# Optimization experiments

Measured on AMD Instinct MI355X. Metric: run time of the kernel, lower is better.

## Reference

```python
import jax, jax.numpy as jnp
import numpy as np

B_, L_, H_ = 2, 2048, 2048          # batch, seq_len, hidden_size
I_, N_, NH, P_ = 4096, 128, 64, 64   # intermediate, ssm_state, num_heads, head_dim
K_, CH = 4, 256                      # conv kernel, chunk size
DT_MIN, DT_MAX = 0.0, 1e10


def setup_inputs() -> dict:
    key = jax.random.key(0)
    ks = jax.random.split(key, 8)
    conv_dim = I_ + 2 * N_
    proj_out = 2 * (I_ + N_) + NH
    return {
        "hidden_states": jax.random.normal(ks[0], (B_, L_, H_), jnp.float32),
        "W_in": jax.random.normal(ks[1], (proj_out, H_), jnp.float32) * 0.02,
        "conv_w": jax.random.normal(ks[2], (conv_dim, 1, K_), jnp.float32) * 0.2,
        "conv_b": jnp.zeros((conv_dim,), jnp.float32),
        "dt_bias": jax.random.uniform(ks[3], (NH,), jnp.float32),
        "A_log": jnp.log(jax.random.uniform(ks[4], (NH,), jnp.float32, 1.0, 16.0)),
        "D": jnp.ones((NH,), jnp.float32),
        "norm_w": jnp.ones((I_,), jnp.float32),
        "W_out": jax.random.normal(ks[5], (H_, I_), jnp.float32) * 0.02,
    }


def _segsum(x):
    # stable segment-sum: out[..., i, j] = sum_{k=j+1..i} x[..., k] for i>=j, else -inf
    T = x.shape[-1]
    xr = jnp.broadcast_to(x[..., None], x.shape + (T,))
    lower = jnp.tril(jnp.ones((T, T), bool), -1)
    s = jnp.cumsum(jnp.where(lower, xr, 0.0), axis=-2)
    return jnp.where(jnp.tril(jnp.ones((T, T), bool)), s, -jnp.inf)


def reference(hidden_states, W_in, conv_w, conv_b, dt_bias, A_log, D, norm_w, W_out):
    b, L, _ = hidden_states.shape
    proj = hidden_states @ W_in.T                       # (b, L, 2*(I+N)+H)
    z, xBC, dt = jnp.split(proj, [I_, 2 * I_ + 2 * N_], axis=-1)

    # depthwise causal conv1d + silu
    x_t = xBC.transpose(0, 2, 1)                        # (b, conv_dim, L)
    conv = jax.lax.conv_general_dilated(
        x_t, conv_w, (1,), [(K_ - 1, 0)],
        dimension_numbers=("NCH", "OIH", "NCH"), feature_group_count=I_ + 2 * N_)
    xBC = jax.nn.silu((conv + conv_b[None, :, None]).transpose(0, 2, 1))
    x, Bm, Cm = jnp.split(xBC, [I_, I_ + N_], axis=-1)  # (b,L,I) (b,L,N) (b,L,N)

    # ---- SSD naive (chunked state-space-duality scan) ----
    A = -jnp.exp(A_log.astype(jnp.float32))             # (h,)
    dt = jnp.clip(jax.nn.softplus(dt + dt_bias), DT_MIN, DT_MAX)  # (b,L,h)
    x4 = x.reshape(b, L, NH, P_)
    pad = (-L) % CH
    padf = lambda t: jnp.pad(t, [(0, 0), (0, pad)] + [(0, 0)] * (t.ndim - 2))
    D_res = D[None, None, :, None] * padf(x4)           # (b, Lp, h, p)
    xs = padf(x4 * dt[..., None])
    Ah = padf(A[None, None, :] * dt)                    # (b, Lp, h)
    Bc, Cc = padf(Bm), padf(Cm)
    c = (L + pad) // CH
    xs = xs.reshape(b, c, CH, NH, P_)                   # (b,c,l,h,p)
    Ah = Ah.reshape(b, c, CH, NH).transpose(0, 3, 1, 2) # (b,h,c,l)
    Bc = Bc.reshape(b, c, CH, N_)
    Cc = Cc.reshape(b, c, CH, N_)

    A_cs = jnp.cumsum(Ah, axis=-1)                      # (b,h,c,l)
    Lm = jnp.exp(_segsum(Ah))                           # (b,h,c,l,l)
    # intra-chunk (diagonal block) output; B/C shared across heads (n_groups=1)
    Y_diag = jnp.einsum("bcln,bcsn,bhcls,bcshp->bclhp", Cc, Bc, Lm, xs)

    decay_states = jnp.exp(A_cs[..., -1:] - A_cs)       # (b,h,c,l)
    states = jnp.einsum("bcln,bhcl,bclhp->bchpn", Bc, decay_states, xs)
    states = jnp.concatenate([jnp.zeros_like(states[:, :1]), states], axis=1)
    decay_chunk = jnp.exp(_segsum(jnp.pad(A_cs[..., -1], [(0, 0), (0, 0), (1, 0)])))
    new_states = jnp.einsum("bhzc,bchpn->bzhpn", decay_chunk, states)
    states = new_states[:, :-1]                         # (b,c,h,p,n)
    Y_off = jnp.einsum("bcln,bchpn,bhcl->bclhp", Cc, states, jnp.exp(A_cs))

    y = (Y_diag + Y_off).reshape(b, c * CH, NH, P_) + D_res
    y = y[:, :L].reshape(b, L, I_)

    # gated RMSNorm (normalize=True: multiply by silu(residual) before norm)
    yf = y.astype(jnp.float32) * jax.nn.silu(z.astype(jnp.float32))
    yf = yf * jax.lax.rsqrt(jnp.mean(yf * yf, -1, keepdims=True) + 1e-5) * norm_w
    return yf.astype(hidden_states.dtype) @ W_out.T
```

## Files before the change

kernel.cpp:

```cpp
#include <hip/hip_runtime.h>
#include <hip/hip_bf16.h>
#include <math.h>


#define B_SZ 2
#define L_SZ 2048
#define H_SZ 2048
#define I_SZ 4096
#define N_SZ 128
#define NH_SZ 64
#define P_SZ 64
#define CH_SZ 256
#define NC_SZ 8
#define PROJ_SZ 8512
#define CONV_SZ 4352
#define XOFF 4096
#define DTOFF 8448
#define BOFF 4096
#define COFF 4224

typedef __attribute__((ext_vector_type(8))) short short8_t;
typedef __attribute__((ext_vector_type(4))) float float4_t;

#define GLDS(gp, lp)                                                   \
// ... 82 lines not shown
                           f2bf(b.x), f2bf(b.y), f2bf(b.z), f2bf(b.w)};
    *(uint4*)(dst + e) = *(const uint4*)o;
  } else {
    *(uint4*)(dst + e) = *(const uint4*)((const unsigned short*)src + e);
  }
}

#define MFMA_ACC(d, a, b) \
  d = __builtin_amdgcn_mfma_f32_16x16x32_bf16(a, b, d, 0, 0, 0)
#define LDA_FR(buf, i, kk) \
  (*(const short8_t*)&As[(buf)*16384 + (wm*128 + (i)*16 + l16)*64 + \
                         (((((kk)<<2) + quad) ^ l7) << 3)])
#define LDB_FR(buf, j, kk) \
  (*(const short8_t*)&Bs[(buf)*16384 + (wn*64 + (j)*16 + l16)*64 + \
                         (((((kk)<<2) + quad) ^ l7) << 3)])
#define STAGE_A(h, tile, buf) do {                                          \
    GLDS(aSrc[h][0] + ((long long)(tile) << 6),                             \
         &As[(buf)*16384 + (h)*8192 + (wave*16)*64]);                       \
    GLDS(aSrc[h][1] + ((long long)(tile) << 6),                             \
         &As[(buf)*16384 + (h)*8192 + (wave*16 + 8)*64]);                   \
  } while (0)
#define STAGE_B(h, tile, buf) do {                                          \
    GLDS(bSrc[h][0] + ((long long)(tile) << 6),                             \
         &Bs[(buf)*16384 + (h)*8192 + (wave*16)*64]);                       \
    GLDS(bSrc[h][1] + ((long long)(tile) << 6),                             \
         &Bs[(buf)*16384 + (h)*8192 + (wave*16 + 8)*64]);                   \
  } while (0)

__global__ __launch_bounds__(512, 2)
void gemm_8ph_k(const unsigned short* __restrict__ A,
                const unsigned short* __restrict__ B,
                unsigned short* __restrict__ C,
                int N, int K, int lda, int ldb, int ldc, int gxTiles) {
  __shared__ alignas(16) unsigned short As[2 * 256 * 64];
  __shared__ alignas(16) unsigned short Bs[2 * 256 * 64];
  const int t = threadIdx.x;
  const int lane = t & 63;
  const int wave = t >> 6;
  const int quad = lane >> 4;
  const int l16 = lane & 15;
  const int l7 = lane & 7;
  const int l3 = lane >> 3;
  const int wm = wave >> 2;
  const int wn = wave & 3;

  int id = blockIdx.x;
  const int nwg = gridDim.x;
  int swz = id;
  if ((nwg & 7) == 0) swz = (id & 7) * (nwg >> 3) + (id >> 3);
  const int band = gxTiles << 2;
  const int by = (swz & 3) + ((swz / band) << 2);
  const int bx = (swz >> 2) % gxTiles;
  const int m0 = by << 8;
  const int n0 = bx << 8;
  const int NT = K >> 6;

  const int kperm = ((l7 ^ l3) << 3);
  const unsigned short* aSrc[2][2];
  const unsigned short* bSrc[2][2];
#pragma unroll
  for (int h = 0; h < 2; ++h)
#pragma unroll
    for (int c = 0; c < 2; ++c) {
      const int rloc = h * 128 + wave * 16 + c * 8 + l3;
      aSrc[h][c] = A + (long long)(m0 + rloc) * lda + kperm;
      int bn = n0 + rloc;
      if (bn > N - 1) bn = N - 1;
      bSrc[h][c] = B + (long long)bn * ldb + kperm;
    }

  float4_t acc[8][4];
#pragma unroll
  for (int i = 0; i < 8; ++i)
#pragma unroll
    for (int j = 0; j < 4; ++j) acc[i][j] = (float4_t){0.f, 0.f, 0.f, 0.f};

  STAGE_A(0, 0, 0); STAGE_A(1, 0, 0);
  STAGE_B(0, 0, 0); STAGE_B(1, 0, 0);
  STAGE_B(0, 1, 1); STAGE_B(1, 1, 1);
  asm volatile("s_waitcnt vmcnt(4)" ::: "memory");
  __builtin_amdgcn_s_barrier();

  short8_t af[4][2], bf[4][2];
  for (int tt = 0; tt < NT; ++tt) {
    const int rb = tt & 1, nb = rb ^ 1;
#pragma unroll
    for (int i = 0; i < 4; ++i) af[i][0] = LDA_FR(rb, i, 0);
#pragma unroll
    for (int j = 0; j < 4; ++j) bf[j][0] = LDB_FR(rb, j, 0);
    if (tt + 1 < NT) STAGE_A(0, tt + 1, nb);
    asm volatile("s_waitcnt lgkmcnt(4)" ::: "memory");
    __builtin_amdgcn_s_barrier();
    asm volatile("s_waitcnt lgkmcnt(0)" ::: "memory");
    __builtin_amdgcn_s_setprio(1);
#pragma unroll
    for (int i = 0; i < 4; ++i)
#pragma unroll
      for (int j = 0; j < 4; ++j) MFMA_ACC(acc[i][j], af[i][0], bf[j][0]);
    __builtin_amdgcn_s_setprio(0);
    __builtin_amdgcn_s_barrier();
#pragma unroll
    for (int i = 0; i < 4; ++i) af[i][1] = LDA_FR(rb, i, 1);
#pragma unroll
    for (int j = 0; j < 4; ++j) bf[j][1] = LDB_FR(rb, j, 1);
    if (tt + 1 < NT) STAGE_A(1, tt + 1, nb);
    asm volatile("s_waitcnt lgkmcnt(4)" ::: "memory");
    __builtin_amdgcn_s_barrier();
    asm volatile("s_waitcnt lgkmcnt(0)" ::: "memory");
    __builtin_amdgcn_s_setprio(1);
#pragma unroll
    for (int i = 0; i < 4; ++i)
#pragma unroll
      for (int j = 0; j < 4; ++j) MFMA_ACC(acc[i][j], af[i][1], bf[j][1]);
    __builtin_amdgcn_s_setprio(0);
    __builtin_amdgcn_s_barrier();
#pragma unroll
    for (int i = 0; i < 4; ++i) af[i][0] = LDA_FR(rb, 4 + i, 0);
    if (tt + 2 < NT) STAGE_B(0, tt + 2, rb);
    __builtin_amdgcn_s_barrier();
    asm volatile("s_waitcnt lgkmcnt(0)" ::: "memory");
    __builtin_amdgcn_s_setprio(1);
#pragma unroll
    for (int i = 0; i < 4; ++i)
#pragma unroll
      for (int j = 0; j < 4; ++j) MFMA_ACC(acc[4 + i][j], af[i][0], bf[j][0]);
    __builtin_amdgcn_s_setprio(0);
    __builtin_amdgcn_s_barrier();
#pragma unroll
    for (int i = 0; i < 4; ++i) af[i][1] = LDA_FR(rb, 4 + i, 1);
    if (tt + 2 < NT) STAGE_B(1, tt + 2, rb);
    __builtin_amdgcn_s_barrier();
    asm volatile("s_waitcnt lgkmcnt(0)" ::: "memory");
    __builtin_amdgcn_s_setprio(1);
#pragma unroll
    for (int i = 0; i < 4; ++i)
#pragma unroll
      for (int j = 0; j < 4; ++j) MFMA_ACC(acc[4 + i][j], af[i][1], bf[j][1]);
    __builtin_amdgcn_s_setprio(0);
    if (tt < NT - 2) asm volatile("s_waitcnt vmcnt(4)" ::: "memory");
    else             asm volatile("s_waitcnt vmcnt(0)" ::: "memory");
    __builtin_amdgcn_s_barrier();
  }

#pragma unroll
  for (int i = 0; i < 8; ++i) {
#pragma unroll
    for (int r = 0; r < 4; ++r) {
      const int m = m0 + wm * 128 + i * 16 + quad * 4 + r;
      const long long cb = (long long)m * ldc;
#pragma unroll
      for (int j = 0; j < 4; ++j) {
        const int n = n0 + wn * 64 + j * 16 + l16;
        if (n < N) C[cb + n] = f2bf(acc[i][j][r]);
      }
    }
  }
}

template <int OUT_MODE>
__global__ __launch_bounds__(256)
void gemm_dma_k(const unsigned short* __restrict__ A,
                const unsigned short* __restrict__ B,
                void* __restrict__ Cptr, int M, int N, int K,
                int lda, int ldb, int ldc,
                const int* __restrict__ flags, int fo) {
  __shared__ unsigned short As[128 * 32];
  __shared__ unsigned short Bs[128 * 32];
  const int t = threadIdx.x;
  const int lane = t & 63;
  const int wave = t >> 6;
  const int quad = lane >> 4;
  const int l16 = lane & 15;
  int bx = blockIdx.x, by = blockIdx.y;
  {
    const int nwg = gridDim.x * gridDim.y;
    if ((nwg & 7) == 0 && (gridDim.y & 3) == 0) {
      int id = blockIdx.y * gridDim.x + blockIdx.x;
      int swz = (id & 7) * (nwg >> 3) + (id >> 3);
      by = (swz & 3) + ((swz / (gridDim.x << 2)) << 2);
      bx = (swz >> 2) % gridDim.x;
    }
  }
  const int m0 = by * 128, n0 = bx * 128;
  const int wm = (wave >> 1) * 64, wn = (wave & 1) * 64;
  const int ofp = (OUT_MODE == 2) ? flags[fo] : 0;

  float4_t acc[4][4];
#pragma unroll
  for (int i = 0; i < 4; i++)
#pragma unroll
    for (int j = 0; j < 4; j++) acc[i][j] = (float4_t){0.f, 0.f, 0.f, 0.f};

  const int rr = lane >> 2;
  const int ks = (lane & 3) * 8;
  const long long aR0 = (long long)(m0 + wave * 16 + rr) * lda + ks;
  const long long aR1 = aR0 + (long long)64 * lda;
  const long long bR0 = (long long)(n0 + wave * 16 + rr) * ldb + ks;
  const long long bR1 = bR0 + (long long)64 * ldb;
  unsigned short* asd0 = &As[(wave * 16) * 32];
  unsigned short* asd1 = &As[(64 + wave * 16) * 32];
  unsigned short* bsd0 = &Bs[(wave * 16) * 32];
  unsigned short* bsd1 = &Bs[(64 + wave * 16) * 32];

  for (int k0 = 0; k0 < K; k0 += 32) {
    __syncthreads();
    GLDS(A + aR0 + k0, asd0);
    GLDS(A + aR1 + k0, asd1);
    GLDS(B + bR0 + k0, bsd0);
    GLDS(B + bR1 + k0, bsd1);
    __syncthreads();
    short8_t afr[4], bfr[4];
#pragma unroll
    for (int i = 0; i < 4; i++)
      afr[i] = *(const short8_t*)&As[(wm + i * 16 + l16) * 32 + quad * 8];
#pragma unroll
    for (int j = 0; j < 4; j++)
      bfr[j] = *(const short8_t*)&Bs[(wn + j * 16 + l16) * 32 + quad * 8];
#pragma unroll
    for (int i = 0; i < 4; i++)
#pragma unroll
      for (int j = 0; j < 4; j++)
        acc[i][j] = __builtin_amdgcn_mfma_f32_16x16x32_bf16(
            afr[i], bfr[j], acc[i][j], 0, 0, 0);
  }
#pragma unroll
  for (int i = 0; i < 4; i++) {
#pragma unroll
    for (int r = 0; r < 4; r++) {
      const int m = m0 + wm + i * 16 + quad * 4 + r;
      const long long base = (long long)m * ldc;
#pragma unroll
      for (int j = 0; j < 4; j++) {
        const int n = n0 + wn + j * 16 + l16;
        if (n < N) {
          float v = acc[i][j][r];
          if (ofp) ((float*)Cptr)[base + n] = v;
          else     ((unsigned short*)Cptr)[base + n] = f2bf(v);
        }
      }
    }
  }
}

template <int OUT_MODE>
__global__ __launch_bounds__(256)
void gemm_bt_k(const void* __restrict__ A, const void* __restrict__ B,
               void* __restrict__ Cptr, int M, int N, int K,
               int lda, int ldb, int ldc,
               long long sA, long long sB, long long sC,
               const int* __restrict__ flags, int fa, int fb, int fo) {
  __shared__ float As[128][20];
  __shared__ float Bs[128][20];
  const int t = threadIdx.x;
  const int tx = t & 15, ty = t >> 4;
  const int m0 = blockIdx.y * 128, n0 = blockIdx.x * 128;
  const int afp = flags[fa], bfp = flags[fb];
  const int ofp = (OUT_MODE == 2) ? flags[fo] : (OUT_MODE == 1);
  const long long zoff = (long long)blockIdx.z;
  float* Cf = (float*)Cptr + zoff * sC;
  unsigned short* Cb = (unsigned short*)Cptr + zoff * sC;

  float acc[8][8];
#pragma unroll
  for (int i = 0; i < 8; i++)
#pragma unroll
    for (int j = 0; j < 8; j++) acc[i][j] = 0.f;

  const int rowS = t >> 1;
  const int kof  = (t & 1) * 8;
  const long long aRow = zoff * sA + (long long)(m0 + rowS) * lda + kof;
  const long long bRow = zoff * sB + (long long)(n0 + rowS) * ldb + kof;
  const bool bOK = (n0 + rowS) < N;

  for (int k0 = 0; k0 < K; k0 += 16) {
    float af[8], bf[8];
    load8(A, aRow + k0, afp, af);
    if (bOK) load8(B, bRow + k0, bfp, bf);
    else { bf[0]=bf[1]=bf[2]=bf[3]=bf[4]=bf[5]=bf[6]=bf[7]=0.f; }
    __syncthreads();
    *(float4*)&As[rowS][kof]     = make_float4(af[0], af[1], af[2], af[3]);
    *(float4*)&As[rowS][kof + 4] = make_float4(af[4], af[5], af[6], af[7]);
    *(float4*)&Bs[rowS][kof]     = make_float4(bf[0], bf[1], bf[2], bf[3]);
    *(float4*)&Bs[rowS][kof + 4] = make_float4(bf[4], bf[5], bf[6], bf[7]);
    __syncthreads();
#pragma unroll
    for (int kk = 0; kk < 16; kk += 2) {
      float2 a2[8], b2[8];
#pragma unroll
      for (int i = 0; i < 8; i++) a2[i] = *(const float2*)&As[ty + 16 * i][kk];
#pragma unroll
      for (int j = 0; j < 8; j++) b2[j] = *(const float2*)&Bs[tx + 16 * j][kk];
#pragma unroll
      for (int i = 0; i < 8; i++)
#pragma unroll
        for (int j = 0; j < 8; j++) {
          acc[i][j] = fmaf(a2[i].x, b2[j].x, acc[i][j]);
          acc[i][j] = fmaf(a2[i].y, b2[j].y, acc[i][j]);
        }
    }
  }
#pragma unroll
  for (int i = 0; i < 8; i++) {
    const int m = m0 + ty + 16 * i;
    const long long base = (long long)m * ldc;
#pragma unroll
    for (int j = 0; j < 8; j++) {
      const int n = n0 + tx + 16 * j;
      if (n < N) {
        if (ofp) Cf[base + n] = acc[i][j];
        else     Cb[base + n] = f2bf(acc[i][j]);
      }
    }
  }
}

__global__ __launch_bounds__(256)
void conv_silu_k(const unsigned short* __restrict__ proj,
                 const void* __restrict__ cw,
                 const void* __restrict__ cb,
                 unsigned short* __restrict__ convx,
                 const int* __restrict__ flags) {
  const int total = B_SZ * L_SZ * (CONV_SZ / 4);
  int g = blockIdx.x * 256 + threadIdx.x;
  if (g >= total) return;
  const int fw = flags[2], fb = flags[3];
  int c4 = g % (CONV_SZ / 4);
  int bl = g / (CONV_SZ / 4);
  int l = bl & (L_SZ - 1);
  int ch = c4 * 4;
  float w0[8], w1[8];
  load8(cw, (long long)ch * 4, fw, w0);
  load8(cw, (long long)ch * 4 + 8, fw, w1);
  float accv[4];
  load4(cb, ch, fb, accv);
  float acc0 = accv[0], acc1 = accv[1], acc2 = accv[2], acc3 = accv[3];
  const long long rb = (long long)(bl - l);
#pragma unroll
  for (int k = 0; k < 4; k++) {
    int ls = l - 3 + k;
    if (ls < 0) continue;
    uint2 xv = *(const uint2*)(proj + (rb + ls) * PROJ_SZ + XOFF + ch);
    float x0 = bf2f((unsigned short)(xv.x & 0xffffu));
    float x1 = bf2f((unsigned short)(xv.x >> 16));
    float x2 = bf2f((unsigned short)(xv.y & 0xffffu));
    float x3 = bf2f((unsigned short)(xv.y >> 16));
    acc0 = fmaf(x0, w0[k], acc0);
    acc1 = fmaf(x1, w0[4 + k], acc1);
    acc2 = fmaf(x2, w1[k], acc2);
    acc3 = fmaf(x3, w1[4 + k], acc3);
  }
  unsigned short o0 = f2bf(silu_f(acc0));
  unsigned short o1 = f2bf(silu_f(acc1));
  unsigned short o2 = f2bf(silu_f(acc2));
  unsigned short o3 = f2bf(silu_f(acc3));
  *(uint2*)(convx + (long long)bl * CONV_SZ + ch) =
      make_uint2((unsigned int)o0 | ((unsigned int)o1 << 16),
                 (unsigned int)o2 | ((unsigned int)o3 << 16));
}

__global__ __launch_bounds__(256)
void dt_prep_k(const unsigned short* __restrict__ proj,
               const void* __restrict__ dt_bias,
               float* __restrict__ dtv, const int* __restrict__ flags) {
  int g = blockIdx.x * 256 + threadIdx.x;
  int h = g & 63;
  long long bl = g >> 6;
  float v = bf2f(proj[bl * PROJ_SZ + DTOFF + h]) + load1(dt_bias, h, flags[4]);
  float sp = (v > 20.f) ? v : log1pf(expf(v));
  dtv[g] = sp;
}

__global__ __launch_bounds__(256)
void acs_scan_k(const float* __restrict__ dtv,
                const void* __restrict__ A_log,
                float* __restrict__ acs, const int* __restrict__ flags) {
  __shared__ float sd[256];
  int blk = blockIdx.x;
  int h = blk & 63;
  int bc = blk >> 6;
  int l = threadIdx.x;
  float Ah = -expf(load1(A_log, h, flags[5]));
  long long row = (long long)bc * CH_SZ + l;
  sd[l] = Ah * dtv[row * NH_SZ + h];
  for (int off = 1; off < 256; off <<= 1) {
    __syncthreads();
    float tv = (l >= off) ? sd[l - off] : 0.f;
    __syncthreads();
    sd[l] += tv;
  }
  acs[(long long)blk * CH_SZ + l] = sd[l];
}

__global__ __launch_bounds__(256)
void chunk_states_k(const unsigned short* __restrict__ convx,
                    const float* __restrict__ dtv,
                    const float* __restrict__ acs,
                    float* __restrict__ stc) {
  __shared__ float Bw[32][128];
  __shared__ float xw[32][64];
  int blk = blockIdx.x;
  int h = blk & 63;
  int bc = blk >> 6;
  int t = threadIdx.x;
  const int p0 = (t & 15) * 4, n0 = (t >> 4) * 8;
  const float* acsb = acs + (long long)blk * 256;
  const float alast = acsb[255];
  float acc[4][8];
#pragma unroll
  for (int i = 0; i < 4; i++)
#pragma unroll
    for (int j = 0; j < 8; j++) acc[i][j] = 0.f;
  const long long row0 = (long long)bc * 256;

  for (int lt0 = 0; lt0 < 256; lt0 += 32) {
    __syncthreads();
#pragma unroll
    for (int q = 0; q < 4; q++) {
      int idx4 = (t + 256 * q) * 4;
      int r = idx4 >> 7, n = idx4 & 127;
      uint2 v = *(const uint2*)(convx + (row0 + lt0 + r) * CONV_SZ + BOFF + n);
      Bw[r][n]     = bf2f((unsigned short)(v.x & 0xffffu));
      Bw[r][n + 1] = bf2f((unsigned short)(v.x >> 16));
      Bw[r][n + 2] = bf2f((unsigned short)(v.y & 0xffffu));
      Bw[r][n + 3] = bf2f((unsigned short)(v.y >> 16));
    }
#pragma unroll
    for (int q = 0; q < 2; q++) {
      int idx4 = (t + 256 * q) * 4;
      int r = idx4 >> 6, p = idx4 & 63;
      long long lg = row0 + lt0 + r;
      float sc = dtv[lg * NH_SZ + h] * expf(alast - acsb[lt0 + r]);
      uint2 v = *(const uint2*)(convx + lg * CONV_SZ + h * 64 + p);
      xw[r][p]     = bf2f((unsigned short)(v.x & 0xffffu)) * sc;
      xw[r][p + 1] = bf2f((unsigned short)(v.x >> 16)) * sc;
      xw[r][p + 2] = bf2f((unsigned short)(v.y & 0xffffu)) * sc;
      xw[r][p + 3] = bf2f((unsigned short)(v.y >> 16)) * sc;
    }
    __syncthreads();
#pragma unroll 4
    for (int lt = 0; lt < 32; lt++) {
      float4 xv = *(const float4*)&xw[lt][p0];
      float4 b0 = *(const float4*)&Bw[lt][n0];
      float4 b1 = *(const float4*)&Bw[lt][n0 + 4];
      float xa[4] = {xv.x, xv.y, xv.z, xv.w};
      float ba[8] = {b0.x, b0.y, b0.z, b0.w, b1.x, b1.y, b1.z, b1.w};
#pragma unroll
      for (int i = 0; i < 4; i++)
#pragma unroll
        for (int j = 0; j < 8; j++) acc[i][j] = fmaf(xa[i], ba[j], acc[i][j]);
    }
  }
  float* outb = stc + (long long)blk * 8192;
#pragma unroll
  for (int i = 0; i < 4; i++) {
    *(float4*)&outb[(p0 + i) * 128 + n0] =
        make_float4(acc[i][0], acc[i][1], acc[i][2], acc[i][3]);
    *(float4*)&outb[(p0 + i) * 128 + n0 + 4] =
        make_float4(acc[i][4], acc[i][5], acc[i][6], acc[i][7]);
  }
}

__global__ __launch_bounds__(256)
void recur_k(float* __restrict__ stc, const float* __restrict__ acs) {
  int blk = blockIdx.x;
  int b = blk >> 6, h = blk & 63;
  int t = threadIdx.x;
  float S[32];
#pragma unroll
  for (int j = 0; j < 32; j++) S[j] = 0.f;
  for (int z = 0; z < 8; z++) {
    long long bz = ((long long)b * 8 + z) * 64 + h;
    long long base = bz * 8192;
    float e = expf(acs[bz * 256 + 255]);
#pragma unroll
    for (int j = 0; j < 32; j++) {
      int idx = j * 256 + t;
      float cs = stc[base + idx];
      stc[base + idx] = S[j];
      S[j] = fmaf(e, S[j], cs);
    }
  }
}

__global__ __launch_bounds__(256)
void yoff_k(const unsigned short* __restrict__ convx,
            const float* __restrict__ sti,
            const float* __restrict__ acs,
            const void* __restrict__ Dw,
            float* __restrict__ y, const int* __restrict__ flags) {
  __shared__ float SIt[128][68];
  __shared__ unsigned short Ct[64][128];
  int blk = blockIdx.x;
  int h = blk & 63;
  int bc = blk >> 6;
  int t = threadIdx.x;
  const int txp = t & 15, lq = t >> 4;
  const float Dh = load1(Dw, h, flags[6]);
  const float* sib = sti + (long long)blk * 8192;
#pragma unroll 4
  for (int q = 0; q < 32; q++) {
    int idx = t + 256 * q;
    SIt[idx & 127][idx >> 7] = sib[idx];
  }
  const float* acsb = acs + (long long)blk * 256;
  const long long row0 = (long long)bc * 256;
  for (int ltile = 0; ltile < 4; ltile++) {
    __syncthreads();
#pragma unroll 4
    for (int q = 0; q < 32; q++) {
      int idx = t + 256 * q;
      int lr = idx >> 7, n = idx & 127;
      Ct[lr][n] = convx[(row0 + ltile * 64 + lr) * CONV_SZ + COFF + n];
    }
    __syncthreads();
    float acc[4][4] = {};
#pragma unroll 4
    for (int n = 0; n < 128; n++) {
      float4 sv = *(const float4*)&SIt[n][txp * 4];
      float c0 = bf2f(Ct[lq * 4 + 0][n]);
      float c1 = bf2f(Ct[lq * 4 + 1][n]);
      float c2 = bf2f(Ct[lq * 4 + 2][n]);
      float c3 = bf2f(Ct[lq * 4 + 3][n]);
      acc[0][0] = fmaf(c0, sv.x, acc[0][0]); acc[0][1] = fmaf(c0, sv.y, acc[0][1]);
      acc[0][2] = fmaf(c0, sv.z, acc[0][2]); acc[0][3] = fmaf(c0, sv.w, acc[0][3]);
      acc[1][0] = fmaf(c1, sv.x, acc[1][0]); acc[1][1] = fmaf(c1, sv.y, acc[1][1]);
      acc[1][2] = fmaf(c1, sv.z, acc[1][2]); acc[1][3] = fmaf(c1, sv.w, acc[1][3]);
      acc[2][0] = fmaf(c2, sv.x, acc[2][0]); acc[2][1] = fmaf(c2, sv.y, acc[2][1]);
      acc[2][2] = fmaf(c2, sv.z, acc[2][2]); acc[2][3] = fmaf(c2, sv.w, acc[2][3]);
      acc[3][0] = fmaf(c3, sv.x, acc[3][0]); acc[3][1] = fmaf(c3, sv.y, acc[3][1]);
      acc[3][2] = fmaf(c3, sv.z, acc[3][2]); acc[3][3] = fmaf(c3, sv.w, acc[3][3]);
    }
#pragma unroll
    for (int i = 0; i < 4; i++) {
      int lloc = ltile * 64 + lq * 4 + i;
      long long row = row0 + lloc;
      float ex = expf(acsb[lloc]);
      uint2 xv = *(const uint2*)(convx + row * CONV_SZ + h * 64 + txp * 4);
      float4 o;
      o.x = fmaf(ex, acc[i][0], Dh * bf2f((unsigned short)(xv.x & 0xffffu)));
      o.y = fmaf(ex, acc[i][1], Dh * bf2f((unsigned short)(xv.x >> 16)));
      o.z = fmaf(ex, acc[i][2], Dh * bf2f((unsigned short)(xv.y & 0xffffu)));
      o.w = fmaf(ex, acc[i][3], Dh * bf2f((unsigned short)(xv.y >> 16)));
      *(float4*)&y[row * I_SZ + h * 64 + txp * 4] = o;
    }
  }
}

__global__ __launch_bounds__(256)
void ydiag_k(const unsigned short* __restrict__ convx,
             const float* __restrict__ dtv,
             const float* __restrict__ acs,
             const float* __restrict__ Gmat,
             float* __restrict__ y) {
  __shared__ float acs_s[256];
  __shared__ float xsT[64][68];
  __shared__ float Mt[64][66];
  int blk = blockIdx.x;
  int h = blk & 63;
  int bc = blk >> 6;
  int t = threadIdx.x;
  const int txp = t & 15, lq = t >> 4;
  acs_s[t] = acs[(long long)blk * 256 + t];
  const long long row0 = (long long)bc * 256;
  const float* Gb = Gmat + (long long)bc * 65536;
  for (int ltile = 0; ltile < 4; ltile++) {
    float acc[4][4] = {};
    for (int stile = 0; stile <= ltile; stile++) {
      __syncthreads();
#pragma unroll 4
      for (int q = 0; q < 16; q++) {
        int idx = t + 256 * q;
        int ss = idx >> 6, p = idx & 63;
        long long row = row0 + stile * 64 + ss;
        xsT[ss][p] = bf2f(convx[row * CONV_SZ + h * 64 + p]) * dtv[row * NH_SZ + h];
      }
#pragma unroll 4
      for (int q = 0; q < 16; q++) {
        int idx = t + 256 * q;
        int lr = idx >> 6, ss = idx & 63;
        int lg = ltile * 64 + lr, sg = stile * 64 + ss;
        float m = 0.f;
        if (sg <= lg) m = Gb[(long long)lg * 256 + sg] * expf(acs_s[lg] - acs_s[sg]);
        Mt[lr][ss] = m;
      }
      __syncthreads();
#pragma unroll 4
      for (int ss = 0; ss < 64; ss++) {
        float4 xv = *(const float4*)&xsT[ss][txp * 4];
        float m0 = Mt[lq * 4 + 0][ss];
        float m1 = Mt[lq * 4 + 1][ss];
        float m2 = Mt[lq * 4 + 2][ss];
        float m3 = Mt[lq * 4 + 3][ss];
        acc[0][0] = fmaf(m0, xv.x, acc[0][0]); acc[0][1] = fmaf(m0, xv.y, acc[0][1]);
        acc[0][2] = fmaf(m0, xv.z, acc[0][2]); acc[0][3] = fmaf(m0, xv.w, acc[0][3]);
        acc[1][0] = fmaf(m1, xv.x, acc[1][0]); acc[1][1] = fmaf(m1, xv.y, acc[1][1]);
        acc[1][2] = fmaf(m1, xv.z, acc[1][2]); acc[1][3] = fmaf(m1, xv.w, acc[1][3]);
        acc[2][0] = fmaf(m2, xv.x, acc[2][0]); acc[2][1] = fmaf(m2, xv.y, acc[2][1]);
        acc[2][2] = fmaf(m2, xv.z, acc[2][2]); acc[2][3] = fmaf(m2, xv.w, acc[2][3]);
        acc[3][0] = fmaf(m3, xv.x, acc[3][0]); acc[3][1] = fmaf(m3, xv.y, acc[3][1]);
        acc[3][2] = fmaf(m3, xv.z, acc[3][2]); acc[3][3] = fmaf(m3, xv.w, acc[3][3]);
      }
    }
#pragma unroll
    for (int i = 0; i < 4; i++) {
      long long row = row0 + ltile * 64 + lq * 4 + i;
      float* yp = &y[row * I_SZ + h * 64 + txp * 4];
      float4 cur = *(float4*)yp;
      cur.x += acc[i][0]; cur.y += acc[i][1]; cur.z += acc[i][2]; cur.w += acc[i][3];
      *(float4*)yp = cur;
    }
  }
}

__global__ __launch_bounds__(256)
void norm_k(const float* __restrict__ y,
            const unsigned short* __restrict__ proj,
            const void* __restrict__ nw,
            unsigned short* __restrict__ yfb, const int* __restrict__ flags) {
  __shared__ float red[4];
  __shared__ float sc_s;
  int row = blockIdx.x;
  int t = threadIdx.x;
  const int fn = flags[7];
  const float* yr = y + (long long)row * I_SZ;
  const unsigned short* zr = proj + (long long)row * PROJ_SZ;
  float g[16];
  float ss = 0.f;
#pragma unroll
  for (int q = 0; q < 4; q++) {
    int i0 = q * 1024 + t * 4;
    float4 yv = *(const float4*)&yr[i0];
    uint2 zv = *(const uint2*)&zr[i0];
    float z0 = bf2f((unsigned short)(zv.x & 0xffffu));
    float z1 = bf2f((unsigned short)(zv.x >> 16));
    float z2 = bf2f((unsigned short)(zv.y & 0xffffu));
    float z3 = bf2f((unsigned short)(zv.y >> 16));
    float g0 = yv.x * silu_f(z0), g1 = yv.y * silu_f(z1);
    float g2 = yv.z * silu_f(z2), g3 = yv.w * silu_f(z3);
    g[q * 4 + 0] = g0; g[q * 4 + 1] = g1; g[q * 4 + 2] = g2; g[q * 4 + 3] = g3;
    ss += g0 * g0 + g1 * g1 + g2 * g2 + g3 * g3;
  }
#pragma unroll
  for (int off = 32; off > 0; off >>= 1) ss += __shfl_down(ss, off, 64);
  if ((t & 63) == 0) red[t >> 6] = ss;
  __syncthreads();
  if (t == 0) sc_s = rsqrtf((red[0] + red[1] + red[2] + red[3]) * (1.f / 4096.f) + 1e-5f);
  __syncthreads();
  float sc = sc_s;
#pragma unroll
  for (int q = 0; q < 4; q++) {
    int i0 = q * 1024 + t * 4;
    float nv[4];
    load4(nw, i0, fn, nv);
    unsigned short o0 = f2bf(g[q * 4 + 0] * sc * nv[0]);
    unsigned short o1 = f2bf(g[q * 4 + 1] * sc * nv[1]);
    unsigned short o2 = f2bf(g[q * 4 + 2] * sc * nv[2]);
    unsigned short o3 = f2bf(g[q * 4 + 3] * sc * nv[3]);
    *(uint2*)&yfb[(long long)row * I_SZ + i0] =
        make_uint2((unsigned int)o0 | ((unsigned int)o1 << 16),
                   (unsigned int)o2 | ((unsigned int)o3 << 16));
  }
}

extern "C" void kernel_launch(void* const* d_in, const int* in_sizes, int n_in,
                              void* d_out, int out_size, void* d_ws, size_t ws_size,
                              hipStream_t stream) {
  const void* hs     = d_in[0];
  const void* W_in   = d_in[1];
  const void* conv_w = d_in[2];
  const void* conv_b = d_in[3];
  const void* dt_b   = d_in[4];
  const void* A_log  = d_in[5];
  const void* Dw     = d_in[6];
  const void* nw     = d_in[7];
  const void* W_out  = d_in[8];

  char* ws = (char*)d_ws;
  size_t off = 0;
  auto alloc = [&](size_t bytes) -> void* {
    void* p = ws + off;
    off += (bytes + 255) & ~(size_t)255;
    return p;
  };
  const long long ML = (long long)B_SZ * L_SZ;
  int* flags = (int*)alloc(64);
  unsigned short* proj  = (unsigned short*)alloc(ML * PROJ_SZ * 2);
  unsigned short* convx = (unsigned short*)alloc(ML * CONV_SZ * 2);
  float* dtv  = (float*)alloc(ML * NH_SZ * 4);
  float* acsb = (float*)alloc((long long)B_SZ * NC_SZ * NH_SZ * CH_SZ * 4);
  float* Gm   = (float*)alloc((long long)B_SZ * NC_SZ * CH_SZ * CH_SZ * 4);
  float* stc  = (float*)alloc((long long)B_SZ * NC_SZ * NH_SZ * P_SZ * N_SZ * 4);
  float* yb   = (float*)alloc(ML * I_SZ * 4);
  unsigned short* yfb = (unsigned short*)stc;
  unsigned short* hs_bf   = (unsigned short*)yb;
  unsigned short* Win_bf  = (unsigned short*)yb + 8388608;
  unsigned short* Wout_bf = (unsigned short*)yb;
  (void)n_in; (void)out_size;
  if (off > ws_size) return;

  dim3 blk(256);
  detect_k<<<1, blk, 0, stream>>>(hs, W_in, conv_w, conv_b, dt_b, A_log, Dw, nw, W_out,
                                  in_sizes[0], in_sizes[1], in_sizes[2], in_sizes[3],
                                  in_sizes[4], in_sizes[5], in_sizes[6], in_sizes[7],
                                  in_sizes[8], flags);
  cvt_bf16_k<<<dim3(4096), blk, 0, stream>>>(hs, hs_bf, 1048576LL, flags, 0);
  cvt_bf16_k<<<dim3(8512), blk, 0, stream>>>(W_in, Win_bf, 2179072LL, flags, 1);
  gemm_8ph_k<<<dim3(512), dim3(512), 0, stream>>>(
      hs_bf, Win_bf, proj, PROJ_SZ, H_SZ, H_SZ, H_SZ, PROJ_SZ, 32);
  gemm_dma_k<0><<<dim3(3, 32), blk, 0, stream>>>(
      hs_bf, Win_bf + 8192LL * 2048, proj + 8192, 4096, 320, H_SZ,
      H_SZ, H_SZ, PROJ_SZ, flags, 15);
  conv_silu_k<<<dim3((B_SZ * L_SZ * (CONV_SZ / 4) + 255) / 256), blk, 0, stream>>>(
      proj, conv_w, conv_b, convx, flags);
  dt_prep_k<<<dim3((unsigned)(ML * NH_SZ / 256)), blk, 0, stream>>>(proj, dt_b, dtv, flags);
  acs_scan_k<<<dim3(B_SZ * NC_SZ * NH_SZ), blk, 0, stream>>>(dtv, A_log, acsb, flags);
  gemm_bt_k<1><<<dim3(2, 2, 16), blk, 0, stream>>>(
      (const unsigned short*)convx + COFF, (const unsigned short*)convx + BOFF,
      Gm, 256, 256, 128, CONV_SZ, CONV_SZ, 256,
      (long long)256 * CONV_SZ, (long long)256 * CONV_SZ, 65536,
      flags, 15, 15, 15);
  chunk_states_k<<<dim3(1024), blk, 0, stream>>>(convx, dtv, acsb, stc);
  recur_k<<<dim3(B_SZ * NH_SZ), blk, 0, stream>>>(stc, acsb);
  yoff_k<<<dim3(1024), blk, 0, stream>>>(convx, stc, acsb, Dw, yb, flags);
  ydiag_k<<<dim3(1024), blk, 0, stream>>>(convx, dtv, acsb, Gm, yb);
  norm_k<<<dim3((unsigned)ML), blk, 0, stream>>>(yb, proj, nw, yfb, flags);
  cvt_bf16_k<<<dim3(4096), blk, 0, stream>>>(W_out, Wout_bf, 1048576LL, flags, 8);
  gemm_dma_k<2><<<dim3(16, 32, 1), blk, 0, stream>>>(
      yfb, Wout_bf, d_out, 4096, H_SZ, I_SZ, I_SZ, I_SZ, H_SZ, flags, 0);
}
```

Measured before the change: 785.8 us.

## Replace output projection GEMM with 512-thread 256x128-tile pipelined kernel

Adds a new GEMM kernel for the final W_out projection. It uses 512-thread blocks with 256x128 output tiles, BK=64, a double-buffered A tile, a triple-buffered B tile staged via direct-to-LDS loads, and XOR-swizzled LDS layout. It also uses an XCD-aware block swizzle and an 8-phase interleave of loads, barriers and MFMA with priority hints. The aim is higher data reuse per block and better overlap of memory traffic with matrix math than the old 128x128 gemm_dma_k. The tradeoffs are larger LDS and register usage and only 256 blocks, which could limit occupancy.

Result: faster. 767.3 us (-2.4%).

```diff
diff --git a/kernel.cpp b/kernel.cpp
--- a/kernel.cpp
+++ b/kernel.cpp
@@ -258,6 +258,146 @@
       for (int j = 0; j < 4; ++j) {
         const int n = n0 + wn * 64 + j * 16 + l16;
         if (n < N) C[cb + n] = f2bf(acc[i][j][r]);
+      }
+    }
+  }
+}
+
+#define LDAH_FR(buf, i, kk) \
+  (*(const short8_t*)&Ah_s[(buf)*16384 + (wmh*64 + (i)*16 + l16)*64 + \
+                           (((((kk)<<2) + quad) ^ l7) << 3)])
+#define LDBH_FR(buf, j, kk) \
+  (*(const short8_t*)&Bh_s[(buf)*8192 + (wnh*64 + (j)*16 + l16)*64 + \
+                           (((((kk)<<2) + quad) ^ l7) << 3)])
+#define STAGEH_A(h, tile, buf) do {                                         \
+    GLDS(aSrc[h][0] + ((long long)(tile) << 6),                             \
+         &Ah_s[(buf)*16384 + ((h)*128 + wave*16)*64]);                      \
+    GLDS(aSrc[h][1] + ((long long)(tile) << 6),                             \
+         &Ah_s[(buf)*16384 + ((h)*128 + wave*16 + 8)*64]);                  \
+  } while (0)
+#define STAGEH_B(tile, buf) do {                                            \
+    GLDS(bSrc[0] + ((long long)(tile) << 6),                                \
+         &Bh_s[(buf)*8192 + (wave*16)*64]);                                 \
+    GLDS(bSrc[1] + ((long long)(tile) << 6),                                \
+         &Bh_s[(buf)*8192 + (wave*16 + 8)*64]);                             \
+  } while (0)
+
+template <int OUT_MODE>
+__global__ __launch_bounds__(512, 2)
+void gemm_8ph_half_k(const unsigned short* __restrict__ A,
+                     const unsigned short* __restrict__ B,
+                     void* __restrict__ Cptr,
+                     int N, int K, int lda, int ldb, int ldc, int gxTiles,
+                     const int* __restrict__ flags, int fo) {
+  __shared__ alignas(16) unsigned short Ah_s[2 * 256 * 64];
+  __shared__ alignas(16) unsigned short Bh_s[3 * 128 * 64];
+  const int t = threadIdx.x;
+  const int lane = t & 63;
+  const int wave = t >> 6;
+  const int quad = lane >> 4;
+  const int l16 = lane & 15;
+  const int l7 = lane & 7;
+  const int l3 = lane >> 3;
+  const int wmh = wave >> 1;
+  const int wnh = wave & 1;
+  const int ofp = (OUT_MODE == 2) ? flags[fo] : 0;
+
+  int id = blockIdx.x;
+  const int nwg = gridDim.x;
+  int swz = id;
+  if ((nwg & 7) == 0) swz = (id & 7) * (nwg >> 3) + (id >> 3);
+  const int band = gxTiles << 2;
+  const int by = (swz & 3) + ((swz / band) << 2);
+  const int bx = (swz >> 2) % gxTiles;
+  const int m0 = by << 8;
+  const int n0 = bx << 7;
+  const int NT = K >> 6;
+
+  const int kperm = ((l7 ^ l3) << 3);
+  const unsigned short* aSrc[2][2];
+  const unsigned short* bSrc[2];
+#pragma unroll
+  for (int h = 0; h < 2; ++h)
+#pragma unroll
+    for (int c = 0; c < 2; ++c) {
+      const int rloc = h * 128 + wave * 16 + c * 8 + l3;
+      aSrc[h][c] = A + (long long)(m0 + rloc) * lda + kperm;
+    }
+#pragma unroll
+  for (int c = 0; c < 2; ++c) {
+    int bn = n0 + wave * 16 + c * 8 + l3;
+    if (bn > N - 1) bn = N - 1;
+    bSrc[c] = B + (long long)bn * ldb + kperm;
+  }
+
+  float4_t acc[4][4];
+#pragma unroll
+  for (int i = 0; i < 4; ++i)
+#pragma unroll
+    for (int j = 0; j < 4; ++j) acc[i][j] = (float4_t){0.f, 0.f, 0.f, 0.f};
+
+  STAGEH_A(0, 0, 0); STAGEH_A(1, 0, 0);
+  STAGEH_B(0, 0);
+  STAGEH_B(1, 1);
+  asm volatile("s_waitcnt vmcnt(2)" ::: "memory");
+  __builtin_amdgcn_s_barrier();
+
+  short8_t af[4], bfr[4];
+  int brb = 0;
+  for (int tt = 0; tt < NT; ++tt) {
+    const int arb = tt & 1, anb = arb ^ 1;
+#pragma unroll
+    for (int i = 0; i < 4; ++i) af[i] = LDAH_FR(arb, i, 0);
+#pragma unroll
+    for (int j = 0; j < 4; ++j) bfr[j] = LDBH_FR(brb, j, 0);
+    if (tt + 1 < NT) { STAGEH_A(0, tt + 1, anb); STAGEH_A(1, tt + 1, anb); }
+    asm volatile("s_waitcnt lgkmcnt(4)" ::: "memory");
+    __builtin_amdgcn_s_barrier();
+    asm volatile("s_waitcnt lgkmcnt(0)" ::: "memory");
+    __builtin_amdgcn_s_setprio(1);
+#pragma unroll
+    for (int i = 0; i < 4; ++i)
+#pragma unroll
+      for (int j = 0; j < 4; ++j) MFMA_ACC(acc[i][j], af[i], bfr[j]);
+    __builtin_amdgcn_s_setprio(0);
+    __builtin_amdgcn_s_barrier();
+#pragma unroll
+    for (int i = 0; i < 4; ++i) af[i] = LDAH_FR(arb, i, 1);
+#pragma unroll
+    for (int j = 0; j < 4; ++j) bfr[j] = LDBH_FR(brb, j, 1);
+    if (tt + 2 < NT) {
+      int b2 = brb + 2; if (b2 >= 3) b2 -= 3;
+      STAGEH_B(tt + 2, b2);
+    }
+    asm volatile("s_waitcnt lgkmcnt(4)" ::: "memory");
+    __builtin_amdgcn_s_barrier();
+    asm volatile("s_waitcnt lgkmcnt(0)" ::: "memory");
+    __builtin_amdgcn_s_setprio(1);
+#pragma unroll
+    for (int i = 0; i < 4; ++i)
+#pragma unroll
+      for (int j = 0; j < 4; ++j) MFMA_ACC(acc[i][j], af[i], bfr[j]);
+    __builtin_amdgcn_s_setprio(0);
+    if (tt < NT - 2) asm volatile("s_waitcnt vmcnt(2)" ::: "memory");
+    else             asm volatile("s_waitcnt vmcnt(0)" ::: "memory");
+    __builtin_amdgcn_s_barrier();
+    ++brb; if (brb == 3) brb = 0;
+  }
+
+#pragma unroll
+  for (int i = 0; i < 4; ++i) {
+#pragma unroll
+    for (int r = 0; r < 4; ++r) {
+      const int m = m0 + wmh * 64 + i * 16 + quad * 4 + r;
+      const long long cb = (long long)m * ldc;
+#pragma unroll
+      for (int j = 0; j < 4; ++j) {
+        const int n = n0 + wnh * 64 + j * 16 + l16;
+        if (n < N) {
+          float v = acc[i][j][r];
+          if (ofp) ((float*)Cptr)[cb + n] = v;
+          else     ((unsigned short*)Cptr)[cb + n] = f2bf(v);
+        }
       }
     }
   }
@@ -831,6 +971,7 @@
   ydiag_k<<<dim3(1024), blk, 0, stream>>>(convx, dtv, acsb, Gm, yb);
   norm_k<<<dim3((unsigned)ML), blk, 0, stream>>>(yb, proj, nw, yfb, flags);
   cvt_bf16_k<<<dim3(4096), blk, 0, stream>>>(W_out, Wout_bf, 1048576LL, flags, 8);
-  gemm_dma_k<2><<<dim3(16, 32, 1), blk, 0, stream>>>(
-      yfb, Wout_bf, d_out, 4096, H_SZ, I_SZ, I_SZ, I_SZ, H_SZ, flags, 0);
-}
+  gemm_8ph_half_k<2><<<dim3(256), dim3(512), 0, stream>>>(
+      yfb, Wout_bf, d_out, H_SZ, I_SZ, I_SZ, I_SZ, H_SZ, 16,
+      flags, 0);
+}
```

## Double-buffer bf16 GEMM with swizzled LDS and fuse Y_off/Y_diag kernels

Applied to the files above, without the earlier changes.

Replaces the single-buffered 32-wide-K DMA GEMM with a 64-wide-K double-buffered version. It uses XOR-swizzled LDS layout, prefetches the next tile during MFMA, and raises wave priority around MFMA. This is used for the small in-projection tail and the output projection. Separately, it merges the Y_off and Y_diag kernels into one, so y is written once instead of written and then read-modified-written. The cost is more LDS per block and shared buffers reused between phases.

Result: no change. 799.8 us (+1.8%).

```diff
diff --git a/kernel.cpp b/kernel.cpp
--- a/kernel.cpp
+++ b/kernel.cpp
@@ -263,85 +263,117 @@
   }
 }
 
+#define LDA2(buf, i, kk) \
+  (*(const short8_t*)&As2[(buf)*8192 + (wm*64 + (i)*16 + l16)*64 + \
+                          (((((kk)<<2) + quad) ^ l7) << 3)])
+#define LDB2(buf, j, kk) \
+  (*(const short8_t*)&Bs2[(buf)*8192 + (wn*64 + (j)*16 + l16)*64 + \
+                          (((((kk)<<2) + quad) ^ l7) << 3)])
+
 template <int OUT_MODE>
-__global__ __launch_bounds__(256)
-void gemm_dma_k(const unsigned short* __restrict__ A,
+__global__ __launch_bounds__(256, 2)
+void gemm_2ph_k(const unsigned short* __restrict__ A,
                 const unsigned short* __restrict__ B,
-                void* __restrict__ Cptr, int M, int N, int K,
-                int lda, int ldb, int ldc,
+                void* __restrict__ Cptr,
+                int N, int K, int lda, int ldb, int ldc, int gxTiles,
                 const int* __restrict__ flags, int fo) {
-  __shared__ unsigned short As[128 * 32];
-  __shared__ unsigned short Bs[128 * 32];
+  __shared__ alignas(16) unsigned short As2[2 * 128 * 64];
+  __shared__ alignas(16) unsigned short Bs2[2 * 128 * 64];
   const int t = threadIdx.x;
   const int lane = t & 63;
   const int wave = t >> 6;
   const int quad = lane >> 4;
   const int l16 = lane & 15;
-  int bx = blockIdx.x, by = blockIdx.y;
-  {
-    const int nwg = gridDim.x * gridDim.y;
-    if ((nwg & 7) == 0 && (gridDim.y & 3) == 0) {
-      int id = blockIdx.y * gridDim.x + blockIdx.x;
-      int swz = (id & 7) * (nwg >> 3) + (id >> 3);
-      by = (swz & 3) + ((swz / (gridDim.x << 2)) << 2);
-      bx = (swz >> 2) % gridDim.x;
-    }
-  }
-  const int m0 = by * 128, n0 = bx * 128;
-  const int wm = (wave >> 1) * 64, wn = (wave & 1) * 64;
+  const int l7 = lane & 7;
+  const int l3 = lane >> 3;
+  const int wm = wave >> 1;
+  const int wn = wave & 1;
   const int ofp = (OUT_MODE == 2) ? flags[fo] : 0;
 
+  int id = blockIdx.x;
+  const int nwg = gridDim.x;
+  int swz = id;
+  if ((nwg & 7) == 0) swz = (id & 7) * (nwg >> 3) + (id >> 3);
+  const int band = gxTiles << 2;
+  const int by = (swz & 3) + ((swz / band) << 2);
+  const int bx = (swz >> 2) % gxTiles;
+  const int m0 = by << 7;
+  const int n0 = bx << 7;
+  const int NT = K >> 6;
+
+  const int kperm = ((l7 ^ l3) << 3);
+  const unsigned short* aSrc[4];
+  const unsigned short* bSrc[4];
+#pragma unroll
+  for (int c = 0; c < 4; ++c) {
+    aSrc[c] = A + (long long)(m0 + wave * 32 + c * 8 + l3) * lda + kperm;
+    int bn = n0 + wave * 32 + c * 8 + l3;
+    if (bn > N - 1) bn = N - 1;
+    bSrc[c] = B + (long long)bn * ldb + kperm;
+  }
+
   float4_t acc[4][4];
 #pragma unroll
-  for (int i = 0; i < 4; i++)
-#pragma unroll
-    for (int j = 0; j < 4; j++) acc[i][j] = (float4_t){0.f, 0.f, 0.f, 0.f};
-
-  const int rr = lane >> 2;
-  const int ks = (lane & 3) * 8;
-  const long long aR0 = (long long)(m0 + wave * 16 + rr) * lda + ks;
-  const long long aR1 = aR0 + (long long)64 * lda;
-  const long long bR0 = (long long)(n0 + wave * 16 + rr) * ldb + ks;
-  const long long bR1 = bR0 + (long long)64 * ldb;
-  unsigned short* asd0 = &As[(wave * 16) * 32];
-  unsigned short* asd1 = &As[(64 + wave * 16) * 32];
-  unsigned short* bsd0 = &Bs[(wave * 16) * 32];
-  unsigned short* bsd1 = &Bs[(64 + wave * 16) * 32];
-
-  for (int k0 = 0; k0 < K; k0 += 32) {
-    __syncthreads();
-    GLDS(A + aR0 + k0, asd0);
-    GLDS(A + aR1 + k0, asd1);
-    GLDS(B + bR0 + k0, bsd0);
-    GLDS(B + bR1 + k0, bsd1);
-    __syncthreads();
-    short8_t afr[4], bfr[4];
-#pragma unroll
-    for (int i = 0; i < 4; i++)
-      afr[i] = *(const short8_t*)&As[(wm + i * 16 + l16) * 32 + quad * 8];
-#pragma unroll
-    for (int j = 0; j < 4; j++)
-      bfr[j] = *(const short8_t*)&Bs[(wn + j * 16 + l16) * 32 + quad * 8];
-#pragma unroll
-    for (int i = 0; i < 4; i++)
-#pragma unroll
-      for (int j = 0; j < 4; j++)
-        acc[i][j] = __builtin_amdgcn_mfma_f32_16x16x32_bf16(
-            afr[i], bfr[j], acc[i][j], 0, 0, 0);
-  }
-#pragma unroll
-  for (int i = 0; i < 4; i++) {
-#pragma unroll
-    for (int r = 0; r < 4; r++) {
-      const int m = m0 + wm + i * 16 + quad * 4 + r;
-      const long long base = (long long)m * ldc;
-#pragma unroll
-      for (int j = 0; j < 4; j++) {
-        const int n = n0 + wn + j * 16 + l16;
+  for (int i = 0; i < 4; ++i)
+#pragma unroll
+    for (int j = 0; j < 4; ++j) acc[i][j] = (float4_t){0.f, 0.f, 0.f, 0.f};
+
+#pragma unroll
+  for (int c = 0; c < 4; ++c) {
+    GLDS(aSrc[c], &As2[(wave * 32 + c * 8) * 64]);
+    GLDS(bSrc[c], &Bs2[(wave * 32 + c * 8) * 64]);
+  }
+  asm volatile("s_waitcnt vmcnt(0)" ::: "memory");
+  __builtin_amdgcn_s_barrier();
+
+  short8_t af[4], bfr[4];
+  for (int tt = 0; tt < NT; ++tt) {
+    const int rb = tt & 1, nb = rb ^ 1;
+#pragma unroll
+    for (int i = 0; i < 4; ++i) af[i] = LDA2(rb, i, 0);
+#pragma unroll
+    for (int j = 0; j < 4; ++j) bfr[j] = LDB2(rb, j, 0);
+    if (tt + 1 < NT) {
+      const long long ko = (long long)(tt + 1) << 6;
+#pragma unroll
+      for (int c = 0; c < 4; ++c) {
+        GLDS(aSrc[c] + ko, &As2[nb * 8192 + (wave * 32 + c * 8) * 64]);
+        GLDS(bSrc[c] + ko, &Bs2[nb * 8192 + (wave * 32 + c * 8) * 64]);
+      }
+    }
+    __builtin_amdgcn_s_setprio(1);
+#pragma unroll
+    for (int i = 0; i < 4; ++i)
+#pragma unroll
+      for (int j = 0; j < 4; ++j) MFMA_ACC(acc[i][j], af[i], bfr[j]);
+    __builtin_amdgcn_s_setprio(0);
+#pragma unroll
+    for (int i = 0; i < 4; ++i) af[i] = LDA2(rb, i, 1);
+#pragma unroll
+    for (int j = 0; j < 4; ++j) bfr[j] = LDB2(rb, j, 1);
+    __builtin_amdgcn_s_setprio(1);
+#pragma unroll
+    for (int i = 0; i < 4; ++i)
+#pragma unroll
+      for (int j = 0; j < 4; ++j) MFMA_ACC(acc[i][j], af[i], bfr[j]);
+    __builtin_amdgcn_s_setprio(0);
+    asm volatile("s_waitcnt vmcnt(0)" ::: "memory");
+    __builtin_amdgcn_s_barrier();
+  }
+
+#pragma unroll
+  for (int i = 0; i < 4; ++i) {
+#pragma unroll
+    for (int r = 0; r < 4; ++r) {
+      const int m = m0 + wm * 64 + i * 16 + quad * 4 + r;
+      const long long cb = (long long)m * ldc;
+#pragma unroll
+      for (int j = 0; j < 4; ++j) {
+        const int n = n0 + wn * 64 + j * 16 + l16;
         if (n < N) {
           float v = acc[i][j][r];
-          if (ofp) ((float*)Cptr)[base + n] = v;
-          else     ((unsigned short*)Cptr)[base + n] = f2bf(v);
+          if (ofp) ((float*)Cptr)[cb + n] = v;
+          else     ((unsigned short*)Cptr)[cb + n] = f2bf(v);
         }
       }
     }
@@ -589,13 +621,20 @@
 }
 
 __global__ __launch_bounds__(256)
-void yoff_k(const unsigned short* __restrict__ convx,
-            const float* __restrict__ sti,
-            const float* __restrict__ acs,
-            const void* __restrict__ Dw,
-            float* __restrict__ y, const int* __restrict__ flags) {
+void yod_k(const unsigned short* __restrict__ convx,
+           const float* __restrict__ sti,
+           const float* __restrict__ acs,
+           const float* __restrict__ dtv,
+           const float* __restrict__ Gmat,
+           const void* __restrict__ Dw,
+           float* __restrict__ y, const int* __restrict__ flags) {
   __shared__ float SIt[128][68];
-  __shared__ unsigned short Ct[64][128];
+  __shared__ float acs_s[256];
+  __shared__ alignas(16) float ubuf[64 * 68 + 64 * 66];
+  float (*xsT)[68] = (float (*)[68])ubuf;
+  float (*Mt)[66]  = (float (*)[66])(ubuf + 64 * 68);
+  unsigned short (*Ct)[128] = (unsigned short (*)[128])ubuf;
+
   int blk = blockIdx.x;
   int h = blk & 63;
   int bc = blk >> 6;
@@ -608,8 +647,10 @@
     int idx = t + 256 * q;
     SIt[idx & 127][idx >> 7] = sib[idx];
   }
-  const float* acsb = acs + (long long)blk * 256;
+  acs_s[t] = acs[(long long)blk * 256 + t];
   const long long row0 = (long long)bc * 256;
+  const float* Gb = Gmat + (long long)bc * 65536;
+
   for (int ltile = 0; ltile < 4; ltile++) {
     __syncthreads();
 #pragma unroll 4
@@ -619,7 +660,7 @@
       Ct[lr][n] = convx[(row0 + ltile * 64 + lr) * CONV_SZ + COFF + n];
     }
     __syncthreads();
-    float acc[4][4] = {};
+    float accO[4][4] = {};
 #pragma unroll 4
     for (int n = 0; n < 128; n++) {
       float4 sv = *(const float4*)&SIt[n][txp * 4];
@@ -627,50 +668,16 @@
       float c1 = bf2f(Ct[lq * 4 + 1][n]);
       float c2 = bf2f(Ct[lq * 4 + 2][n]);
       float c3 = bf2f(Ct[lq * 4 + 3][n]);
-      acc[0][0] = fmaf(c0, sv.x, acc[0][0]); acc[0][1] = fmaf(c0, sv.y, acc[0][1]);
-      acc[0][2] = fmaf(c0, sv.z, acc[0][2]); acc[0][3] = fmaf(c0, sv.w, acc[0][3]);
-      acc[1][0] = fmaf(c1, sv.x, acc[1][0]); acc[1][1] = fmaf(c1, sv.y, acc[1][1]);
-      acc[1][2] = fmaf(c1, sv.z, acc[1][2]); acc[1][3] = fmaf(c1, sv.w, acc[1][3]);
-      acc[2][0] = fmaf(c2, sv.x, acc[2][0]); acc[2][1] = fmaf(c2, sv.y, acc[2][1]);
-      acc[2][2] = fmaf(c2, sv.z, acc[2][2]); acc[2][3] = fmaf(c2, sv.w, acc[2][3]);
-      acc[3][0] = fmaf(c3, sv.x, acc[3][0]); acc[3][1] = fmaf(c3, sv.y, acc[3][1]);
-      acc[3][2] = fmaf(c3, sv.z, acc[3][2]); acc[3][3] = fmaf(c3, sv.w, acc[3][3]);
-    }
-#pragma unroll
-    for (int i = 0; i < 4; i++) {
-      int lloc = ltile * 64 + lq * 4 + i;
-      long long row = row0 + lloc;
-      float ex = expf(acsb[lloc]);
-      uint2 xv = *(const uint2*)(convx + row * CONV_SZ + h * 64 + txp * 4);
-      float4 o;
-      o.x = fmaf(ex, acc[i][0], Dh * bf2f((unsigned short)(xv.x & 0xffffu)));
-      o.y = fmaf(ex, acc[i][1], Dh * bf2f((unsigned short)(xv.x >> 16)));
-      o.z = fmaf(ex, acc[i][2], Dh * bf2f((unsigned short)(xv.y & 0xffffu)));
-      o.w = fmaf(ex, acc[i][3], Dh * bf2f((unsigned short)(xv.y >> 16)));
-      *(float4*)&y[row * I_SZ + h * 64 + txp * 4] = o;
-    }
-  }
-}
-
-__global__ __launch_bounds__(256)
-void ydiag_k(const unsigned short* __restrict__ convx,
-             const float* __restrict__ dtv,
-             const float* __restrict__ acs,
-             const float* __restrict__ Gmat,
-             float* __restrict__ y) {
-  __shared__ float acs_s[256];
-  __shared__ float xsT[64][68];
-  __shared__ float Mt[64][66];
-  int blk = blockIdx.x;
-  int h = blk & 63;
-  int bc = blk >> 6;
-  int t = threadIdx.x;
-  const int txp = t & 15, lq = t >> 4;
-  acs_s[t] = acs[(long long)blk * 256 + t];
-  const long long row0 = (long long)bc * 256;
-  const float* Gb = Gmat + (long long)bc * 65536;
-  for (int ltile = 0; ltile < 4; ltile++) {
-    float acc[4][4] = {};
+      accO[0][0] = fmaf(c0, sv.x, accO[0][0]); accO[0][1] = fmaf(c0, sv.y, accO[0][1]);
+      accO[0][2] = fmaf(c0, sv.z, accO[0][2]); accO[0][3] = fmaf(c0, sv.w, accO[0][3]);
+      accO[1][0] = fmaf(c1, sv.x, accO[1][0]); accO[1][1] = fmaf(c1, sv.y, accO[1][1]);
+      accO[1][2] = fmaf(c1, sv.z, accO[1][2]); accO[1][3] = fmaf(c1, sv.w, accO[1][3]);
+      accO[2][0] = fmaf(c2, sv.x, accO[2][0]); accO[2][1] = fmaf(c2, sv.y, accO[2][1]);
+      accO[2][2] = fmaf(c2, sv.z, accO[2][2]); accO[2][3] = fmaf(c2, sv.w, accO[2][3]);
+      accO[3][0] = fmaf(c3, sv.x, accO[3][0]); accO[3][1] = fmaf(c3, sv.y, accO[3][1]);
+      accO[3][2] = fmaf(c3, sv.z, accO[3][2]); accO[3][3] = fmaf(c3, sv.w, accO[3][3]);
+    }
+    float accD[4][4] = {};
     for (int stile = 0; stile <= ltile; stile++) {
       __syncthreads();
 #pragma unroll 4
@@ -697,23 +704,28 @@
         float m1 = Mt[lq * 4 + 1][ss];
         float m2 = Mt[lq * 4 + 2][ss];
         float m3 = Mt[lq * 4 + 3][ss];
-        acc[0][0] = fmaf(m0, xv.x, acc[0][0]); acc[0][1] = fmaf(m0, xv.y, acc[0][1]);
-        acc[0][2] = fmaf(m0, xv.z, acc[0][2]); acc[0][3] = fmaf(m0, xv.w, acc[0][3]);
-        acc[1][0] = fmaf(m1, xv.x, acc[1][0]); acc[1][1] = fmaf(m1, xv.y, acc[1][1]);
-        acc[1][2] = fmaf(m1, xv.z, acc[1][2]); acc[1][3] = fmaf(m1, xv.w, acc[1][3]);
-        acc[2][0] = fmaf(m2, xv.x, acc[2][0]); acc[2][1] = fmaf(m2, xv.y, acc[2][1]);
-        acc[2][2] = fmaf(m2, xv.z, acc[2][2]); acc[2][3] = fmaf(m2, xv.w, acc[2][3]);
-        acc[3][0] = fmaf(m3, xv.x, acc[3][0]); acc[3][1] = fmaf(m3, xv.y, acc[3][1]);
-        acc[3][2] = fmaf(m3, xv.z, acc[3][2]); acc[3][3] = fmaf(m3, xv.w, acc[3][3]);
+        accD[0][0] = fmaf(m0, xv.x, accD[0][0]); accD[0][1] = fmaf(m0, xv.y, accD[0][1]);
+        accD[0][2] = fmaf(m0, xv.z, accD[0][2]); accD[0][3] = fmaf(m0, xv.w, accD[0][3]);
+        accD[1][0] = fmaf(m1, xv.x, accD[1][0]); accD[1][1] = fmaf(m1, xv.y, accD[1][1]);
+        accD[1][2] = fmaf(m1, xv.z, accD[1][2]); accD[1][3] = fmaf(m1, xv.w, accD[1][3]);
+        accD[2][0] = fmaf(m2, xv.x, accD[2][0]); accD[2][1] = fmaf(m2, xv.y, accD[2][1]);
+        accD[2][2] = fmaf(m2, xv.z, accD[2][2]); accD[2][3] = fmaf(m2, xv.w, accD[2][3]);
+        accD[3][0] = fmaf(m3, xv.x, accD[3][0]); accD[3][1] = fmaf(m3, xv.y, accD[3][1]);
+        accD[3][2] = fmaf(m3, xv.z, accD[3][2]); accD[3][3] = fmaf(m3, xv.w, accD[3][3]);
       }
     }
 #pragma unroll
     for (int i = 0; i < 4; i++) {
-      long long row = row0 + ltile * 64 + lq * 4 + i;
-      float* yp = &y[row * I_SZ + h * 64 + txp * 4];
-      float4 cur = *(float4*)yp;
-      cur.x += acc[i][0]; cur.y += acc[i][1]; cur.z += acc[i][2]; cur.w += acc[i][3];
-      *(float4*)yp = cur;
+      int lloc = ltile * 64 + lq * 4 + i;
+      long long row = row0 + lloc;
+      float ex = expf(acs_s[lloc]);
+      uint2 xv = *(const uint2*)(convx + row * CONV_SZ + h * 64 + txp * 4);
+      float4 o;
+      o.x = fmaf(ex, accO[i][0], Dh * bf2f((unsigned short)(xv.x & 0xffffu))) + accD[i][0];
+      o.y = fmaf(ex, accO[i][1], Dh * bf2f((unsigned short)(xv.x >> 16)))     + accD[i][1];
+      o.z = fmaf(ex, accO[i][2], Dh * bf2f((unsigned short)(xv.y & 0xffffu))) + accD[i][2];
+      o.w = fmaf(ex, accO[i][3], Dh * bf2f((unsigned short)(xv.y >> 16)))     + accD[i][3];
+      *(float4*)&y[row * I_SZ + h * 64 + txp * 4] = o;
     }
   }
 }
@@ -813,9 +825,9 @@
   cvt_bf16_k<<<dim3(8512), blk, 0, stream>>>(W_in, Win_bf, 2179072LL, flags, 1);
   gemm_8ph_k<<<dim3(512), dim3(512), 0, stream>>>(
       hs_bf, Win_bf, proj, PROJ_SZ, H_SZ, H_SZ, H_SZ, PROJ_SZ, 32);
-  gemm_dma_k<0><<<dim3(3, 32), blk, 0, stream>>>(
-      hs_bf, Win_bf + 8192LL * 2048, proj + 8192, 4096, 320, H_SZ,
-      H_SZ, H_SZ, PROJ_SZ, flags, 15);
+  gemm_2ph_k<0><<<dim3(96), blk, 0, stream>>>(
+      hs_bf, Win_bf + 8192LL * 2048, proj + 8192, 320, H_SZ,
+      H_SZ, H_SZ, PROJ_SZ, 3, flags, 15);
   conv_silu_k<<<dim3((B_SZ * L_SZ * (CONV_SZ / 4) + 255) / 256), blk, 0, stream>>>(
       proj, conv_w, conv_b, convx, flags);
   dt_prep_k<<<dim3((unsigned)(ML * NH_SZ / 256)), blk, 0, stream>>>(proj, dt_b, dtv, flags);
@@ -827,10 +839,10 @@
       flags, 15, 15, 15);
   chunk_states_k<<<dim3(1024), blk, 0, stream>>>(convx, dtv, acsb, stc);
   recur_k<<<dim3(B_SZ * NH_SZ), blk, 0, stream>>>(stc, acsb);
-  yoff_k<<<dim3(1024), blk, 0, stream>>>(convx, stc, acsb, Dw, yb, flags);
-  ydiag_k<<<dim3(1024), blk, 0, stream>>>(convx, dtv, acsb, Gm, yb);
+  yod_k<<<dim3(1024), blk, 0, stream>>>(convx, stc, acsb, dtv, Gm, Dw, yb, flags);
   norm_k<<<dim3((unsigned)ML), blk, 0, stream>>>(yb, proj, nw, yfb, flags);
   cvt_bf16_k<<<dim3(4096), blk, 0, stream>>>(W_out, Wout_bf, 1048576LL, flags, 8);
-  gemm_dma_k<2><<<dim3(16, 32, 1), blk, 0, stream>>>(
-      yfb, Wout_bf, d_out, 4096, H_SZ, I_SZ, I_SZ, I_SZ, H_SZ, flags, 0);
-}
+  gemm_2ph_k<2><<<dim3(512), blk, 0, stream>>>(
+      yfb, Wout_bf, d_out, H_SZ, I_SZ, I_SZ, I_SZ, H_SZ, 16,
+      flags, 0);
+}
```
